# Kernel optimization log

Hardware: AMD Instinct MI355X
Metric: run time of the kernel (lower is better)

The kernel has to match this reference:

```python
import jax, jax.numpy as jnp
import numpy as np

# ---- db4 filters (pywt conventions: dec_lo = rec_lo[::-1], rec_hi = qmf(rec_lo)) ----
F = 8  # db4 filter length
_rec_lo = np.array([0.23037781330885523, 0.7148465705525415, 0.6308807679295904,
                    -0.027983769416983849, -0.18703481171888114, 0.030841381835986965,
                    0.032883011666982945, -0.010597401784997278], dtype=np.float32)
_rec_hi = _rec_lo[::-1].copy()
_rec_hi[1::2] *= -1.0
REC_LO = jnp.asarray(_rec_lo)
REC_HI = jnp.asarray(_rec_hi)

MAX_LEVEL = 9  # pywt.dwt_max_level(4096, 8)


def _conv1d(x, kernel, stride=1, padding='VALID', lhs_dilation=None):
    # x: [B, L] -> correlation (XLA conv does NOT flip the kernel)
    out = jax.lax.conv_general_dilated(
        x[:, None, :], kernel[None, None, :],
        window_strides=(stride,), padding=padding,
        lhs_dilation=lhs_dilation,
        dimension_numbers=('NCH', 'OIH', 'NCH'))
    return out[:, 0, :]


def dwt(x):
    # pywt.dwt(x, 'db4', mode='symmetric'):
    # cA = np.convolve(sym_ext(x, F-1), dec_lo, 'valid')[1::2]
    # convolution with dec filter == correlation with rec filter (its reverse)
    ext = jnp.pad(x, ((0, 0), (F - 1, F - 1)), mode='symmetric')[:, 1:]
    return _conv1d(ext, REC_LO, stride=2), _conv1d(ext, REC_HI, stride=2)


def idwt(ca, cd):
    # pywt.idwt: zero-upsample coeffs, full convolution with rec filters, trim edges
    n = ca.shape[1]
    pad = ((F - 1, F - 1),)
    out = (_conv1d(ca, REC_LO[::-1], padding=pad, lhs_dilation=(2,)) +
           _conv1d(cd, REC_HI[::-1], padding=pad, lhs_dilation=(2,)))
    return out[:, F - 2:2 * n]  # output length = 2n - F + 2


def wavelet_features(x1):
    # Faithful to WaveletDWTLayer stack + WaveletParsingLayer: at each level k>=2,
    # reconstruct with details of levels k and k-1 only (others zeroed), with
    # pywt.waverec's trim-by-one rule; concatenate the 8 full-length reconstructions.
    a = x1
    cds, recs = [], []
    for level in range(1, MAX_LEVEL + 1):
        a, d = dwt(a)
        if level >= 2:
            r = idwt(jnp.zeros_like(d), d)
            for j in range(level - 2, -1, -1):
                dj = cds[j] if j == level - 2 else jnp.zeros_like(cds[j])
                if r.shape[1] == dj.shape[1] + 1:  # waverec trim rule
                    r = r[:, :-1]
                r = idwt(r, dj)
            recs.append(r)  # [B, signal_length]
        cds.append(d)
    return jnp.concatenate(recs, axis=1)  # [B, signal_length*(MAX_LEVEL-1)]


def reference(x1, x2, x3, W0, b0, W1, b1, W2, b2):
    # x2/x3 are placeholders in the original module (overwritten by layers 1/2)
    h = wavelet_features(x1)
    for W, b in ((W0, b0), (W1, b1), (W2, b2)):
        h = jax.nn.relu(h) @ W.T + b
    return h


def setup_inputs() -> dict:
    key = jax.random.key(0)
    ks = jax.random.split(key, 4)
    B, N = 2048, 4096
    D_IN, H1, H2, OUT = 32768, 181, 13, 10
    return {
        'x1': jax.random.normal(ks[0], (B, N), jnp.float32),
        'x2': jnp.zeros((B, 1, 8), jnp.float32),
        'x3': jnp.zeros((B, 1, 8), jnp.float32),
        'W0': jax.random.normal(ks[1], (H1, D_IN), jnp.float32) / np.float32(np.sqrt(D_IN)),
        'b0': jnp.zeros((H1,), jnp.float32),
        'W1': jax.random.normal(ks[2], (H2, H1), jnp.float32) / np.float32(np.sqrt(H1)),
        'b1': jnp.zeros((H2,), jnp.float32),
        'W2': jax.random.normal(ks[3], (OUT, H2), jnp.float32) / np.float32(np.sqrt(H2)),
        'b2': jnp.zeros((OUT,), jnp.float32),
    }
```

## Files before the change

kernel.cpp:

```cpp
#include <hip/hip_runtime.h>
#include <hip/hip_bf16.h>


typedef _Float16 f16x8 __attribute__((ext_vector_type(8)));
typedef _Float16 f16x4v __attribute__((ext_vector_type(4)));
typedef float f32x4 __attribute__((ext_vector_type(4)));

#define WV_THREADS 256
#define DROW 4144

#define L0 0.23037781330885523f
#define L1 0.7148465705525415f
#define L2f 0.6308807679295904f
#define L3 -0.02798376941698385f
#define L4 -0.18703481171888114f
#define L5 0.030841381835986965f
#define L6 0.032883011666982945f
#define L7 -0.010597401784997278f

#define H0 -0.010597401784997278f
#define H1 -0.032883011666982945f
#define H2 0.030841381835986965f
#define H3 0.18703481171888114f
#define H4 -0.02798376941698385f
#define H5 -0.6308807679295904f
#define H6 0.7148465705525415f
#define H7 -0.23037781330885523f

__device__ __forceinline__ int ext_idx(int j, int n) {
  return (j < 6) ? (5 - j) : ((j < n + 6) ? (j - 6) : (2 * n + 5 - j));
}

__device__ __forceinline__ void dwt2(const float* a, float* anext, float* d,
                                     int n, int m, bool store_a) {
  const int ng = (m + 1) >> 1;
  for (int g = threadIdx.x; g < ng; g += WV_THREADS) {
    float w[10];
    if (g >= 2 && 4 * g + 9 <= n + 5) {
      const float2* af = (const float2*)a + (2 * g - 3);
      float2 b0 = af[0], b1 = af[1], b2 = af[2], b3 = af[3], b4 = af[4];
      w[0] = b0.x; w[1] = b0.y; w[2] = b1.x; w[3] = b1.y; w[4] = b2.x;
      w[5] = b2.y; w[6] = b3.x; w[7] = b3.y; w[8] = b4.x; w[9] = b4.y;
    } else {
#pragma unroll
      for (int q = 0; q < 10; ++q) {
        int j = 4 * g + q;
        int jm = n + 12;
        if (j > jm) j = jm;
        w[q] = a[ext_idx(j, n)];
      }
    }
    float sl0 = w[0]*L0 + w[1]*L1 + w[2]*L2f + w[3]*L3 + w[4]*L4 + w[5]*L5 + w[6]*L6 + w[7]*L7;
    float sh0 = w[0]*H0 + w[1]*H1 + w[2]*H2  + w[3]*H3 + w[4]*H4 + w[5]*H5 + w[6]*H6 + w[7]*H7;
    float sl1 = w[2]*L0 + w[3]*L1 + w[4]*L2f + w[5]*L3 + w[6]*L4 + w[7]*L5 + w[8]*L6 + w[9]*L7;
    float sh1 = w[2]*H0 + w[3]*H1 + w[4]*H2  + w[5]*H3 + w[6]*H4 + w[7]*H5 + w[8]*H6 + w[9]*H7;
    if (2 * g + 1 < m) {
      if (store_a) *(float2*)(anext + 2 * g) = make_float2(sl0, sl1);
      *(float2*)(d + 2 * g) = make_float2(sh0, sh1);
    } else {
      if (store_a) anext[2 * g] = sl0;
      d[2 * g] = sh0;
    }
  }
}

template <bool HAS_CA, bool HAS_CD, bool FINAL>
__device__ __forceinline__ void idwt2(const float* ca, const float* cd,
                                      float* outl, _Float16* outg, int dlen) {
  const int npair = dlen - 3;
  const int ng = (npair + 1) >> 1;
  for (int g = threadIdx.x; g < ng; g += WV_THREADS) {
    float e0 = 0.f, o0 = 0.f, e1 = 0.f, o1 = 0.f;
    if (HAS_CA) {
      const float2* f = (const float2*)ca + g;
      float2 a0 = f[0], a1 = f[1], a2 = f[2];
      e0 = a1.y*L0 + a1.x*L2f + a0.y*L4 + a0.x*L6;
      o0 = a1.y*L1 + a1.x*L3  + a0.y*L5 + a0.x*L7;
      e1 = a2.x*L0 + a1.y*L2f + a1.x*L4 + a0.y*L6;
      o1 = a2.x*L1 + a1.y*L3  + a1.x*L5 + a0.y*L7;
    }
    if (HAS_CD) {
      const float2* f = (const float2*)cd + g;
      float2 d0 = f[0], d1 = f[1], d2 = f[2];
      e0 += d1.y*H0 + d1.x*H2 + d0.y*H4 + d0.x*H6;
      o0 += d1.y*H1 + d1.x*H3 + d0.y*H5 + d0.x*H7;
      e1 += d2.x*H0 + d1.y*H2 + d1.x*H4 + d0.y*H6;
      o1 += d2.x*H1 + d1.y*H3 + d1.x*H5 + d0.y*H7;
    }
    bool full = (2 * g + 1 < npair);
    if (FINAL) {
      if (full) {
        f16x4v h;
        h[0] = (_Float16)fmaxf(e0, 0.f); h[1] = (_Float16)fmaxf(o0, 0.f);
        h[2] = (_Float16)fmaxf(e1, 0.f); h[3] = (_Float16)fmaxf(o1, 0.f);
        *(f16x4v*)(outg + 4 * g) = h;
      } else {
        outg[4 * g]     = (_Float16)fmaxf(e0, 0.f);
        outg[4 * g + 1] = (_Float16)fmaxf(o0, 0.f);
      }
    } else {
      if (full) *(float4*)(outl + 4 * g) = make_float4(e0, o0, e1, o1);
      else      *(float2*)(outl + 4 * g) = make_float2(e0, o0);
    }
  }
}

__global__ __launch_bounds__(WV_THREADS) void wv_analysis(
    const float* __restrict__ x, float* __restrict__ dG) {
  __shared__ float r1[4104];
  __shared__ float r2[2056];
  const int NLa[10]  = {4096, 2051, 1029, 518, 262, 134, 70, 38, 22, 14};
  const int DOFF[10] = {0, 0, 2052, 3082, 3600, 3862, 3996, 4066, 4104, 4126};
  const int row = blockIdx.x;
  const int tid = threadIdx.x;

  const float4* xr = (const float4*)(x + (size_t)row * 4096);
  for (int i = tid; i < 1024; i += WV_THREADS) ((float4*)r1)[i] = xr[i];
  __syncthreads();

  float* dr = dG + (size_t)row * DROW;
  const float* ap = r1;
  float* an = r2;
  for (int lev = 1; lev <= 9; ++lev) {
    dwt2(ap, an, dr + DOFF[lev], NLa[lev - 1], NLa[lev], lev < 9);
    __syncthreads();
    const float* t = ap; ap = an; an = (float*)t;
  }
}

__global__ __launch_bounds__(WV_THREADS, 6) void wv_synth(
    const float* __restrict__ dG, _Float16* __restrict__ A) {
  __shared__ float s1[2052];
  __shared__ float s2[2052];
  const int NLa[10]  = {4096, 2051, 1029, 518, 262, 134, 70, 38, 22, 14};
  const int DOFF[10] = {0, 0, 2052, 3082, 3600, 3862, 3996, 4066, 4104, 4126};
  const int row = blockIdx.x;
  const int L = 2 + blockIdx.y;
  const float* dr = dG + (size_t)row * DROW;

  idwt2<false, true, false>(nullptr, dr + DOFF[L], s1, nullptr, NLa[L]);
  __syncthreads();
  float* cur = s1;
  float* nxt = s2;
  for (int j = L - 2; j >= 1; --j) {
    if (j == L - 2)
      idwt2<true, true, false>(cur, dr + DOFF[j + 1], nxt, nullptr, NLa[j + 1]);
    else
      idwt2<true, false, false>(cur, nullptr, nxt, nullptr, NLa[j + 1]);
    __syncthreads();
    float* t = cur; cur = nxt; nxt = t;
  }
  _Float16* og = A + (size_t)row * 32768 + (size_t)(L - 2) * 4096;
  if (L == 2)
    idwt2<true, true, true>(cur, dr + DOFF[1], nullptr, og, 2051);
  else
    idwt2<true, false, true>(cur, nullptr, nullptr, og, 2051);
}

__global__ __launch_bounds__(256) void cvt_w0(const float* __restrict__ W0,
                                              _Float16* __restrict__ Bw) {
  size_t i = ((size_t)blockIdx.x * 256 + threadIdx.x) * 4;
  int rowc = (int)(i >> 15);
  f16x4v h;
  if (rowc < 181) {
    const float4 v = *(const float4*)(W0 + i);
    h[0] = (_Float16)v.x; h[1] = (_Float16)v.y;
    h[2] = (_Float16)v.z; h[3] = (_Float16)v.w;
  } else {
    h[0] = (_Float16)0.f; h[1] = (_Float16)0.f;
    h[2] = (_Float16)0.f; h[3] = (_Float16)0.f;
  }
  *(f16x4v*)(Bw + i) = h;
}

__device__ __forceinline__ void load_lds16(const void* g, void* l) {
  __builtin_amdgcn_global_load_lds((__attribute__((address_space(1))) unsigned int*)g,
                                   (__attribute__((address_space(3))) unsigned int*)l,
                                   16, 0, 0);
}

__global__ __launch_bounds__(256, 2) void gemm_kernel(
    const _Float16* __restrict__ A, const _Float16* __restrict__ Bw,
    float* __restrict__ P, int kchunk) {
  __shared__ _Float16 As[128 * 64];
  __shared__ _Float16 Bs[192 * 64];
  const int tid = threadIdx.x;
  const int lane = tid & 63;
  const int wave = tid >> 6;
  const int m0 = blockIdx.x * 128;
  const int k0 = blockIdx.y * kchunk;
  const int nstages = kchunk >> 6;

  f32x4 acc[2][12];
#pragma unroll
  for (int mt = 0; mt < 2; ++mt)
#pragma unroll
    for (int nt = 0; nt < 12; ++nt) acc[mt][nt] = (f32x4){0.f, 0.f, 0.f, 0.f};

  for (int ks = 0; ks < nstages; ++ks) {
    const int kbase = k0 + (ks << 6);
    __syncthreads();
#pragma unroll
    for (int t = 0; t < 4; ++t) {
      int g = ((wave * 4 + t) << 6) + lane;
      int r = g >> 3, cs = g & 7;
      const _Float16* gp = A + (size_t)(m0 + r) * 32768 + kbase + ((cs ^ (r & 7)) << 3);
      load_lds16(gp, (char*)As + (size_t)((wave * 4 + t) << 10));
    }
#pragma unroll
    for (int t = 0; t < 6; ++t) {
      int g = ((wave * 6 + t) << 6) + lane;
      int r = g >> 3, cs = g & 7;
      const _Float16* gp = Bw + (size_t)r * 32768 + kbase + ((cs ^ (r & 7)) << 3);
      load_lds16(gp, (char*)Bs + (size_t)((wave * 6 + t) << 10));
    }
    __syncthreads();
#pragma unroll
    for (int kk = 0; kk < 2; ++kk) {
      const int chunk = kk * 4 + (lane >> 4);
      f16x8 af[2];
#pragma unroll
      for (int mt = 0; mt < 2; ++mt) {
        int r = wave * 32 + mt * 16 + (lane & 15);
        af[mt] = *(const f16x8*)(As + r * 64 + ((chunk ^ (r & 7)) << 3));
      }
#pragma unroll
      for (int nt = 0; nt < 12; ++nt) {
        int rb = nt * 16 + (lane & 15);
        f16x8 bf = *(const f16x8*)(Bs + rb * 64 + ((chunk ^ (rb & 7)) << 3));
        acc[0][nt] = __builtin_amdgcn_mfma_f32_16x16x32_f16(af[0], bf, acc[0][nt], 0, 0, 0);
        acc[1][nt] = __builtin_amdgcn_mfma_f32_16x16x32_f16(af[1], bf, acc[1][nt], 0, 0, 0);
      }
    }
  }
  float* Pp = P + ((size_t)blockIdx.y * 2048 + m0) * 192;
#pragma unroll
  for (int mt = 0; mt < 2; ++mt)
#pragma unroll
    for (int nt = 0; nt < 12; ++nt)
#pragma unroll
      for (int r4 = 0; r4 < 4; ++r4) {
        int rr = wave * 32 + mt * 16 + ((lane >> 4) << 2) + r4;
        int cc = nt * 16 + (lane & 15);
        Pp[(size_t)rr * 192 + cc] = acc[mt][nt][r4];
      }
}

__global__ __launch_bounds__(256) void mlp_kernel(
    const float* __restrict__ P, const float* __restrict__ b0,
    const float* __restrict__ W1, const float* __restrict__ b1,
    const float* __restrict__ W2, const float* __restrict__ b2,
    float* __restrict__ out, int nsplit) {
  __shared__ float h1[181];
  __shared__ float h2[13];
  const int row = blockIdx.x;
  const int t = threadIdx.x;
  if (t < 181) {
    float c = b0[t];
    for (int s = 0; s < nsplit; ++s)
      c += P[((size_t)s * 2048 + row) * 192 + t];
    h1[t] = fmaxf(c, 0.f);
  }
  __syncthreads();
  if (t < 13) {
    float c = b1[t];
    for (int n = 0; n < 181; ++n) c += h1[n] * W1[t * 181 + n];
    h2[t] = fmaxf(c, 0.f);
  }
  __syncthreads();
  if (t < 10) {
    float c = b2[t];
    for (int j = 0; j < 13; ++j) c += h2[j] * W2[t * 13 + j];
    out[(size_t)row * 10 + t] = c;
  }
}

extern "C" void kernel_launch(void* const* d_in, const int* in_sizes, int n_in,
                              void* d_out, int out_size, void* d_ws, size_t ws_size,
                              hipStream_t stream) {
  const float* x1 = (const float*)d_in[0];
  const float* W0 = (const float*)d_in[3];
  const float* b0 = (const float*)d_in[4];
  const float* W1 = (const float*)d_in[5];
  const float* b1 = (const float*)d_in[6];
  const float* W2 = (const float*)d_in[7];
  const float* b2 = (const float*)d_in[8];
  float* out = (float*)d_out;

  char* ws = (char*)d_ws;
  const size_t A_BYTES = (size_t)2048 * 32768 * 2;
  const size_t B_BYTES = (size_t)192 * 32768 * 2;
  _Float16* Afeat = (_Float16*)ws;
  _Float16* Bw = (_Float16*)(ws + A_BYTES);
  float* Dq = (float*)(ws + A_BYTES + B_BYTES);
  float* P = (float*)(ws + A_BYTES + B_BYTES);

  int nsplit = 32;
  while (nsplit > 1 &&
         A_BYTES + B_BYTES + (size_t)nsplit * 2048 * 192 * 4 > ws_size)
    nsplit >>= 1;

  cvt_w0<<<6144, 256, 0, stream>>>(W0, Bw);
  wv_analysis<<<2048, WV_THREADS, 0, stream>>>(x1, Dq);
  dim3 sg(2048, 8);
  wv_synth<<<sg, WV_THREADS, 0, stream>>>(Dq, Afeat);
  dim3 gg(16, nsplit);
  gemm_kernel<<<gg, 256, 0, stream>>>(Afeat, Bw, P, 32768 / nsplit);
  mlp_kernel<<<2048, 256, 0, stream>>>(P, b0, W1, b1, W2, b2, out, nsplit);
}
```

Baseline: 242.8 us.

## Fuse W0 conversion into analysis kernel, stage details in LDS, parallelize MLP

Merges the W0 fp16 conversion into the wavelet analysis launch as extra blocks, removing one kernel launch. Level 2-9 detail coefficients are first kept in spare shared memory and then written to global memory together, instead of being stored inside each level. In synthesis, the small early levels for L>=6 are run by a single wave without block barriers. The MLP kernel now spreads the split-K partial sums over all four waves and computes layer 2 with wave shuffles, at the cost of more shared memory and extra code complexity.

```diff
diff --git a/kernel.cpp b/kernel.cpp
--- a/kernel.cpp
+++ b/kernel.cpp
@@ -105,26 +105,53 @@
   }
 }
 
-__global__ __launch_bounds__(WV_THREADS) void wv_analysis(
-    const float* __restrict__ x, float* __restrict__ dG) {
+__global__ __launch_bounds__(WV_THREADS) void wv_analysis_cvt(
+    const float* __restrict__ x, float* __restrict__ dG,
+    const float* __restrict__ W0, _Float16* __restrict__ Bw) {
   __shared__ float r1[4104];
   __shared__ float r2[2056];
+  const int tid = threadIdx.x;
+
+  if (blockIdx.x >= 2048) {
+    size_t i = ((size_t)(blockIdx.x - 2048) * 256 + tid) * 4;
+    int rowc = (int)(i >> 15);
+    f16x4v h;
+    if (rowc < 181) {
+      const float4 v = *(const float4*)(W0 + i);
+      h[0] = (_Float16)v.x; h[1] = (_Float16)v.y;
+      h[2] = (_Float16)v.z; h[3] = (_Float16)v.w;
+    } else {
+      h[0] = (_Float16)0.f; h[1] = (_Float16)0.f;
+      h[2] = (_Float16)0.f; h[3] = (_Float16)0.f;
+    }
+    *(f16x4v*)(Bw + i) = h;
+    return;
+  }
+
   const int NLa[10]  = {4096, 2051, 1029, 518, 262, 134, 70, 38, 22, 14};
   const int DOFF[10] = {0, 0, 2052, 3082, 3600, 3862, 3996, 4066, 4104, 4126};
+  const int LOFF[10] = {0, 0, 1036, 520, 2068, 1040, 2332, 1176, 2404, 1216};
   const int row = blockIdx.x;
-  const int tid = threadIdx.x;
 
   const float4* xr = (const float4*)(x + (size_t)row * 4096);
   for (int i = tid; i < 1024; i += WV_THREADS) ((float4*)r1)[i] = xr[i];
   __syncthreads();
 
   float* dr = dG + (size_t)row * DROW;
-  const float* ap = r1;
-  float* an = r2;
-  for (int lev = 1; lev <= 9; ++lev) {
-    dwt2(ap, an, dr + DOFF[lev], NLa[lev - 1], NLa[lev], lev < 9);
+  dwt2(r1, r2, dr + DOFF[1], NLa[0], NLa[1], true);
+  __syncthreads();
+  const float* ap = r2;
+  float* an = r1;
+  for (int lev = 2; lev <= 9; ++lev) {
+    float* dbuf = ((lev & 1) ? r2 : r1) + LOFF[lev];
+    dwt2(ap, an, dbuf, NLa[lev - 1], NLa[lev], lev < 9);
     __syncthreads();
     const float* t = ap; ap = an; an = (float*)t;
+  }
+  for (int lev = 2; lev <= 9; ++lev) {
+    const float* src = ((lev & 1) ? r2 : r1) + LOFF[lev];
+    float* dst = dr + DOFF[lev];
+    for (int i = tid; i < NLa[lev]; i += WV_THREADS) dst[i] = src[i];
   }
 }
 
@@ -136,13 +163,34 @@
   const int DOFF[10] = {0, 0, 2052, 3082, 3600, 3862, 3996, 4066, 4104, 4126};
   const int row = blockIdx.x;
   const int L = 2 + blockIdx.y;
+  const int tid = threadIdx.x;
   const float* dr = dG + (size_t)row * DROW;
 
-  idwt2<false, true, false>(nullptr, dr + DOFF[L], s1, nullptr, NLa[L]);
-  __syncthreads();
   float* cur = s1;
   float* nxt = s2;
-  for (int j = L - 2; j >= 1; --j) {
+  int startj = L - 2;
+  if (L >= 6) {
+    if (tid < 64) {
+      idwt2<false, true, false>(nullptr, dr + DOFF[L], cur, nullptr, NLa[L]);
+      asm volatile("s_waitcnt lgkmcnt(0)" ::: "memory");
+      for (int j = L - 2; j >= 5; --j) {
+        if (j == L - 2)
+          idwt2<true, true, false>(cur, dr + DOFF[j + 1], nxt, nullptr, NLa[j + 1]);
+        else
+          idwt2<true, false, false>(cur, nullptr, nxt, nullptr, NLa[j + 1]);
+        asm volatile("s_waitcnt lgkmcnt(0)" ::: "memory");
+        float* t = cur; cur = nxt; nxt = t;
+      }
+    } else {
+      for (int j = L - 2; j >= 5; --j) { float* t = cur; cur = nxt; nxt = t; }
+    }
+    __syncthreads();
+    startj = 4;
+  } else {
+    idwt2<false, true, false>(nullptr, dr + DOFF[L], cur, nullptr, NLa[L]);
+    __syncthreads();
+  }
+  for (int j = startj; j >= 1; --j) {
     if (j == L - 2)
       idwt2<true, true, false>(cur, dr + DOFF[j + 1], nxt, nullptr, NLa[j + 1]);
     else
@@ -155,22 +203,6 @@
     idwt2<true, true, true>(cur, dr + DOFF[1], nullptr, og, 2051);
   else
     idwt2<true, false, true>(cur, nullptr, nullptr, og, 2051);
-}
-
-__global__ __launch_bounds__(256) void cvt_w0(const float* __restrict__ W0,
-                                              _Float16* __restrict__ Bw) {
-  size_t i = ((size_t)blockIdx.x * 256 + threadIdx.x) * 4;
-  int rowc = (int)(i >> 15);
-  f16x4v h;
-  if (rowc < 181) {
-    const float4 v = *(const float4*)(W0 + i);
-    h[0] = (_Float16)v.x; h[1] = (_Float16)v.y;
-    h[2] = (_Float16)v.z; h[3] = (_Float16)v.w;
-  } else {
-    h[0] = (_Float16)0.f; h[1] = (_Float16)0.f;
-    h[2] = (_Float16)0.f; h[3] = (_Float16)0.f;
-  }
-  *(f16x4v*)(Bw + i) = h;
 }
 
 __device__ __forceinline__ void load_lds16(const void* g, void* l) {
@@ -251,25 +283,49 @@
     const float* __restrict__ W1, const float* __restrict__ b1,
     const float* __restrict__ W2, const float* __restrict__ b2,
     float* __restrict__ out, int nsplit) {
-  __shared__ float h1[181];
+  __shared__ float part[4][193];
+  __shared__ float h1[192];
   __shared__ float h2[13];
   const int row = blockIdx.x;
   const int t = threadIdx.x;
-  if (t < 181) {
-    float c = b0[t];
-    for (int s = 0; s < nsplit; ++s)
-      c += P[((size_t)s * 2048 + row) * 192 + t];
-    h1[t] = fmaxf(c, 0.f);
-  }
-  __syncthreads();
-  if (t < 13) {
-    float c = b1[t];
-    for (int n = 0; n < 181; ++n) c += h1[n] * W1[t * 181 + n];
-    h2[t] = fmaxf(c, 0.f);
-  }
-  __syncthreads();
+  const int g = t >> 6;
+  const int l = t & 63;
+
+  float a0 = 0.f, a1 = 0.f, a2 = 0.f;
+  const int per = nsplit >> 2;
+  for (int si = 0; si < per; ++si) {
+    int s = g + (si << 2);
+    const float* Pr = P + ((size_t)s * 2048 + row) * 192;
+    a0 += Pr[l]; a1 += Pr[64 + l]; a2 += Pr[128 + l];
+  }
+  part[g][l] = a0; part[g][64 + l] = a1; part[g][128 + l] = a2;
+  __syncthreads();
+
+  if (t < 192) {
+    float v = part[0][t] + part[1][t] + part[2][t] + part[3][t];
+    h1[t] = (t < 181) ? fmaxf(v + b0[t], 0.f) : 0.f;
+  }
+  __syncthreads();
+
+#pragma unroll
+  for (int r = 0; r < 4; ++r) {
+    int j = g + (r << 2);
+    if (j < 13) {
+      float v = 0.f;
+#pragma unroll
+      for (int q = 0; q < 3; ++q) {
+        int n = l + (q << 6);
+        if (n < 181) v += h1[n] * W1[j * 181 + n];
+      }
+      for (int off = 32; off >= 1; off >>= 1) v += __shfl_down(v, off);
+      if (l == 0) h2[j] = fmaxf(v + b1[j], 0.f);
+    }
+  }
+  __syncthreads();
+
   if (t < 10) {
     float c = b2[t];
+#pragma unroll
     for (int j = 0; j < 13; ++j) c += h2[j] * W2[t * 13 + j];
     out[(size_t)row * 10 + t] = c;
   }
@@ -300,8 +356,7 @@
          A_BYTES + B_BYTES + (size_t)nsplit * 2048 * 192 * 4 > ws_size)
     nsplit >>= 1;
 
-  cvt_w0<<<6144, 256, 0, stream>>>(W0, Bw);
-  wv_analysis<<<2048, WV_THREADS, 0, stream>>>(x1, Dq);
+  wv_analysis_cvt<<<2048 + 6144, WV_THREADS, 0, stream>>>(x1, Dq, W0, Bw);
   dim3 sg(2048, 8);
   wv_synth<<<sg, WV_THREADS, 0, stream>>>(Dq, Afeat);
   dim3 gg(16, nsplit);
```

Measured after the change: 228.2 us. -6.0%, faster.
